# Performance work log

Measured on AMD Instinct MI355X. Metric: run time of the kernel, lower is better.

Reference implementation:

```python
import jax, jax.numpy as jnp
import numpy as np
from jax import lax

B, D, N, C = 8, 1, 12288, 256
H = 8            # num_heads
WS = 64          # window size (pixels per window)
HID = 1024       # mlp hidden = 4*C
K = 9            # conv kernel size
EPS = 1e-5


def setup_inputs() -> dict:
    key = jax.random.key(0)
    ks = jax.random.split(key, 8)
    w = lambda i, shape: jax.random.normal(ks[i], shape, jnp.float32) * 0.02
    return {
        "x": jax.random.normal(ks[0], (B, D, N, C), jnp.float32),
        "ln1_g": jnp.ones((C,), jnp.float32),
        "ln1_b": jnp.zeros((C,), jnp.float32),
        "conv_w": w(1, (C, C, K)),            # OIH layout (out_ch, in_ch, k)
        "conv_b": jnp.zeros((C,), jnp.float32),
        "qkv_w": w(2, (C, 3 * C)),            # stored (in, out): y = x @ W + b
        "qkv_b": jnp.zeros((3 * C,), jnp.float32),
        "proj_w": w(3, (C, C)),
        "proj_b": jnp.zeros((C,), jnp.float32),
        "ln2_g": jnp.ones((C,), jnp.float32),
        "ln2_b": jnp.zeros((C,), jnp.float32),
        "fc1_w": w(4, (C, HID)),
        "fc1_b": jnp.zeros((HID,), jnp.float32),
        "fc2_w": w(5, (HID, C)),
        "fc2_b": jnp.zeros((C,), jnp.float32),
    }


def _layernorm(x, g, b):
    mu = jnp.mean(x, axis=-1, keepdims=True)
    var = jnp.mean(jnp.square(x - mu), axis=-1, keepdims=True)
    return (x - mu) * lax.rsqrt(var + EPS) * g + b


def reference(x, ln1_g, ln1_b, conv_w, conv_b, qkv_w, qkv_b,
              proj_w, proj_b, ln2_g, ln2_b, fc1_w, fc1_b, fc2_w, fc2_b):
    shortcut = x                                  # (B, D, N, C)
    h = _layernorm(x, ln1_g, ln1_b)

    # Conv1d over pixel dim N, channels C, same padding
    hc = h.reshape(B * D, N, C).transpose(0, 2, 1)            # (BD, C, N)
    hc = lax.conv_general_dilated(
        hc, conv_w, window_strides=(1,), padding=[((K - 1) // 2, (K - 1) // 2)],
        dimension_numbers=("NCH", "OIH", "NCH"))
    hc = hc + conv_b[None, :, None]
    h = hc.transpose(0, 2, 1).reshape(B, D, N, C)

    # Window partition (no shift): (B*D*N/WS, WS, C)
    win = h.reshape(-1, WS, C)
    hd = C // H
    qkv = (win @ qkv_w + qkv_b).reshape(-1, WS, 3, H, hd)
    q = qkv[:, :, 0].transpose(0, 2, 1, 3)        # (nW, H, WS, hd)
    k = qkv[:, :, 1].transpose(0, 2, 1, 3)
    v = qkv[:, :, 2].transpose(0, 2, 1, 3)
    scale = hd ** (-0.5)
    attn = jnp.einsum("whqd,whkd->whqk", q * scale, k)
    attn = jax.nn.softmax(attn, axis=-1)
    out = jnp.einsum("whqk,whkd->whqd", attn, v)
    out = out.transpose(0, 2, 1, 3).reshape(-1, WS, C)
    out = out @ proj_w + proj_b

    h = out.reshape(B, D, N, C)
    x1 = shortcut + h                             # residual 1
    mlp_in = _layernorm(x1, ln2_g, ln2_b)
    mlp = jax.nn.gelu(mlp_in @ fc1_w + fc1_b, approximate=False) @ fc2_w + fc2_b
    return x1 + mlp                               # residual 2
```

## Files before the change

### kernel.cpp

```cpp
#include <hip/hip_runtime.h>

#define DEVI __device__ __forceinline__

typedef __attribute__((ext_vector_type(4))) float  f32x4;
typedef __attribute__((ext_vector_type(8))) short  s16x8;
typedef __attribute__((ext_vector_type(4))) short  s16x4;
typedef __attribute__((ext_vector_type(8))) __bf16 bf16x8;

constexpr int  Nn  = 12288;
constexpr int  NP  = 12296;
constexpr long TOK = 98304;

DEVI short f2bf(float f) {
  unsigned u = __builtin_bit_cast(unsigned, f);
  u += 0x7fffu + ((u >> 16) & 1u);
  return (short)(u >> 16);
}

DEVI f32x4 MFMA(s16x8 a, s16x8 b, f32x4 c) {
  return __builtin_amdgcn_mfma_f32_16x16x32_bf16(
      __builtin_bit_cast(bf16x8, a), __builtin_bit_cast(bf16x8, b), c, 0, 0, 0);
}

DEVI void gld16(const void* g, void* l) {
  __builtin_amdgcn_global_load_lds(
      (const __attribute__((address_space(1))) void*)g,
      (__attribute__((address_space(3))) void*)l, 16, 0, 0);
}

template <int CNT, int NT>
DEVI void stageG(const short* __restrict__ g_base, long g_row0, int ld, int k0,
                 short* __restrict__ lds, int tid) {
  const int w = tid >> 6;
#pragma unroll
  for (int c = 0; c < CNT; ++c) {
    const int u = c * NT + tid;
    const int row = u >> 3, ch = u & 7;
    const short* g = g_base + (g_row0 + row) * (long)ld + k0 + ch * 8;
    gld16(g, lds + (c * NT + w * 64) * 8);
  }
}

DEVI void xcd_decode(int W, int total, int ncol, long& row0, int& col0) {
  const int per = total >> 3;
  const int L = (W & 7) * per + (W >> 3);
  row0 = (long)(L / ncol) * 128;
  col0 = (L % ncol) * 128;
}

__global__ void prep_k(const float* __restrict__ qkv_w, const float* __restrict__ proj_w,
                       const float* __restrict__ fc1_w, const float* __restrict__ fc2_w,
                       const float* __restrict__ conv_w,
                       short* __restrict__ qkvWt, short* __restrict__ projWt,
                       short* __restrict__ fc1Wt, short* __restrict__ fc2Wt,
                       short* __restrict__ convWt, short* __restrict__ hp) {
  int idx = blockIdx.x * 256 + threadIdx.x;
  if (idx < 196608) {
    int o = idx >> 8, i = idx & 255;
    qkvWt[idx] = f2bf(qkv_w[i * 768 + o]);
    return;
  }
  idx -= 196608;
  if (idx < 65536) {
    int o = idx >> 8, i = idx & 255;
    projWt[idx] = f2bf(proj_w[i * 256 + o]);
    return;
  }
  idx -= 65536;
  if (idx < 262144) {
    int o = idx >> 8, i = idx & 255;
    fc1Wt[idx] = f2bf(fc1_w[i * 1024 + o]);
    return;
  }
  idx -= 262144;
  if (idx < 262144) {
    int o = idx >> 10, i = idx & 1023;
    fc2Wt[idx] = f2bf(fc2_w[i * 256 + o]);
    return;
  }
  idx -= 262144;
  if (idx < 589824) {
    int co = idx / 2304, rem = idx % 2304;
    int k = rem >> 8, ci = rem & 255;
    convWt[idx] = f2bf(conv_w[co * 2304 + ci * 9 + k]);
    return;
  }
  idx -= 589824;
  if (idx < 16384) {
    int b = idx >> 11, rem = idx & 2047;
    int rs = rem >> 8, ch = rem & 255;
    int p = rs < 4 ? rs : 12288 + rs;
    hp[((long)b * NP + p) * 256 + ch] = 0;
  }
}

__global__ __launch_bounds__(256) void ln_k(const float* __restrict__ x,
                                            const float* __restrict__ gw,
                                            const float* __restrict__ bw,
                                            short* __restrict__ out) {
  const int tid = threadIdx.x, w = tid >> 6, lane = tid & 63;
  const long t = (long)blockIdx.x * 4 + w;
  f32x4 v = *((const f32x4*)(x + t * 256) + lane);
  float s  = v[0] + v[1] + v[2] + v[3];
  float ss = v[0] * v[0] + v[1] * v[1] + v[2] * v[2] + v[3] * v[3];
#pragma unroll
  for (int mk = 1; mk < 64; mk <<= 1) {
    s  += __shfl_xor(s, mk);
    ss += __shfl_xor(ss, mk);
  }
  const float mu   = s * (1.0f / 256.0f);
  const float var  = ss * (1.0f / 256.0f) - mu * mu;
  const float rstd = rsqrtf(var + 1e-5f);
  f32x4 g4 = *((const f32x4*)gw + lane);
  f32x4 b4 = *((const f32x4*)bw + lane);
  const long orow = t + (t / Nn) * 8 + 4;
  s16x4 o4;
#pragma unroll
  for (int j = 0; j < 4; ++j) o4[j] = f2bf((v[j] - mu) * rstd * g4[j] + b4[j]);
  *((s16x4*)(out + orow * 256) + lane) = o4;
}

template <int EPI>
__global__ __launch_bounds__(256, 2) void gemm_k(
    const short* __restrict__ A, int lda,
    const short* __restrict__ Bt,
    const float* __restrict__ bias,
    const float* res, short* outS, float* outF,
    int ldo, int K, int ncol) {
  __shared__ __align__(16) short As[2][128][64];
  __shared__ __align__(16) short Bs[2][128][64];
  const int tid = threadIdx.x, w = tid >> 6, lane = tid & 63;
  const int q = lane >> 4, r16 = lane & 15;
  long row0; int col0;
  xcd_decode(blockIdx.x, gridDim.x, ncol, row0, col0);
  const int wr = w >> 1, wc = w & 1;
  f32x4 acc[4][4] = {};

  stageG<4, 256>(A, row0, lda, 0, &As[0][0][0], tid);
  stageG<4, 256>(Bt, col0, K, 0, &Bs[0][0][0], tid);
  __syncthreads();
  int cur = 0;
  for (int k0 = 0; k0 < K; k0 += 64) {
    if (k0 + 64 < K) {
      stageG<4, 256>(A, row0, lda, k0 + 64, &As[cur ^ 1][0][0], tid);
      stageG<4, 256>(Bt, col0, K, k0 + 64, &Bs[cur ^ 1][0][0], tid);
    }
#pragma unroll
    for (int kk = 0; kk < 2; ++kk) {
      s16x8 af[4], bfv[4];
#pragma unroll
      for (int m = 0; m < 4; ++m) af[m] = *(const s16x8*)&As[cur][wr * 64 + m * 16 + r16][kk * 32 + q * 8];
#pragma unroll
      for (int n = 0; n < 4; ++n) bfv[n] = *(const s16x8*)&Bs[cur][wc * 64 + n * 16 + r16][kk * 32 + q * 8];
#pragma unroll
      for (int m = 0; m < 4; ++m)
#pragma unroll
        for (int n = 0; n < 4; ++n) acc[m][n] = MFMA(af[m], bfv[n], acc[m][n]);
    }
    __syncthreads();
    cur ^= 1;
  }

  const long orow = row0 + wr * 64;
  const int  ocol = col0 + wc * 64;
#pragma unroll
  for (int n = 0; n < 4; ++n) {
    const int   gc = ocol + n * 16 + r16;
    const float bn = bias[gc];
#pragma unroll
    for (int m = 0; m < 4; ++m) {
      const long gr = orow + m * 16 + q * 4;
#pragma unroll
      for (int r = 0; r < 4; ++r) {
        float v = acc[m][n][r] + bn;
        const long o = (gr + r) * (long)ldo + gc;
        if constexpr (EPI == 0) {
          outS[o] = f2bf(v);
        } else if constexpr (EPI == 1) {
          outF[o] = v + res[o];
        } else {
          float t = 0.5f * v * (1.0f + erff(v * 0.70710678118654752f));
          outS[o] = f2bf(t);
        }
      }
    }
  }
}

__global__ __launch_bounds__(256, 2) void conv_k(const short* __restrict__ hp,
                                                 const short* __restrict__ convWt,
                                                 const float* __restrict__ bias,
                                                 short* __restrict__ out) {
  __shared__ __align__(16) short As[160][64];
  __shared__ __align__(16) short Bs[2][128][64];
  const int tid = threadIdx.x, w = tid >> 6, lane = tid & 63;
  const int q = lane >> 4, r16 = lane & 15;
  long row0; int col0;
  xcd_decode(blockIdx.x, gridDim.x, 2, row0, col0);
  const int  b  = (int)(row0 / Nn);
  const int  n0 = (int)(row0 % Nn);
  const long abase = (long)b * NP + n0;
  const int  wr = w >> 1, wc = w & 1;
  f32x4 acc[4][4] = {};

  stageG<5, 256>(hp, abase, 256, 0, &As[0][0], tid);
  stageG<4, 256>(convWt, col0, 2304, 0, &Bs[0][0][0], tid);
  __syncthreads();
  int cur = 0;
  for (int k0 = 0; k0 < 256; k0 += 64) {
    for (int tap = 0; tap < 9; ++tap) {
      if (tap < 8)
        stageG<4, 256>(convWt, col0, 2304, (tap + 1) * 256 + k0, &Bs[cur ^ 1][0][0], tid);
      else if (k0 + 64 < 256)
        stageG<4, 256>(convWt, col0, 2304, k0 + 64, &Bs[cur ^ 1][0][0], tid);
#pragma unroll
      for (int kk = 0; kk < 2; ++kk) {
        s16x8 af[4], bfv[4];
#pragma unroll
        for (int m = 0; m < 4; ++m)
          af[m] = *(const s16x8*)&As[tap + wr * 64 + m * 16 + r16][kk * 32 + q * 8];
#pragma unroll
        for (int n = 0; n < 4; ++n)
          bfv[n] = *(const s16x8*)&Bs[cur][wc * 64 + n * 16 + r16][kk * 32 + q * 8];
#pragma unroll
        for (int m = 0; m < 4; ++m)
#pragma unroll
          for (int n = 0; n < 4; ++n) acc[m][n] = MFMA(af[m], bfv[n], acc[m][n]);
      }
      __syncthreads();
      cur ^= 1;
    }
    if (k0 + 64 < 256) {
      stageG<5, 256>(hp, abase, 256, k0 + 64, &As[0][0], tid);
      __syncthreads();
    }
  }

  const long orow = row0 + wr * 64;
  const int  ocol = col0 + wc * 64;
#pragma unroll
  for (int n = 0; n < 4; ++n) {
    const int   gc = ocol + n * 16 + r16;
    const float bn = bias[gc];
#pragma unroll
    for (int m = 0; m < 4; ++m) {
      const long gr = orow + m * 16 + q * 4;
#pragma unroll
      for (int r = 0; r < 4; ++r) out[(gr + r) * 256L + gc] = f2bf(acc[m][n][r] + bn);
    }
  }
}

__global__ __launch_bounds__(512, 4) void proj_ln_k(
    const short* __restrict__ A,
    const short* __restrict__ Bt,
    const float* __restrict__ bias,
    const float* __restrict__ res,
    const float* __restrict__ gw, const float* __restrict__ bw,
    float* __restrict__ x1,
    short* __restrict__ lnout) {
  __shared__ __align__(16) short As[128][64];
  __shared__ __align__(16) short Bs[256][64];
  __shared__ float red[4][128][2];
  const int tid = threadIdx.x, w = tid >> 6, lane = tid & 63;
  const int q = lane >> 4, r16 = lane & 15;
  const int W = blockIdx.x, per = gridDim.x >> 3;
  const long row0 = (long)((W & 7) * per + (W >> 3)) * 128;
  const int wr = w >> 2, wc = w & 3;
  f32x4 acc[4][4] = {};

  for (int k0 = 0; k0 < 256; k0 += 64) {
    stageG<2, 512>(A, row0, 256, k0, &As[0][0], tid);
    stageG<4, 512>(Bt, 0, 256, k0, &Bs[0][0], tid);
    __syncthreads();
#pragma unroll
    for (int kk = 0; kk < 2; ++kk) {
      s16x8 af[4], bfv[4];
#pragma unroll
      for (int m = 0; m < 4; ++m) af[m] = *(const s16x8*)&As[wr * 64 + m * 16 + r16][kk * 32 + q * 8];
#pragma unroll
      for (int n = 0; n < 4; ++n) bfv[n] = *(const s16x8*)&Bs[wc * 64 + n * 16 + r16][kk * 32 + q * 8];
#pragma unroll
      for (int m = 0; m < 4; ++m)
#pragma unroll
        for (int n = 0; n < 4; ++n) acc[m][n] = MFMA(af[m], bfv[n], acc[m][n]);
    }
    __syncthreads();
  }

  float biasr[4], gv[4], bv[4];
#pragma unroll
  for (int n = 0; n < 4; ++n) {
    const int gc = wc * 64 + n * 16 + r16;
    biasr[n] = bias[gc]; gv[n] = gw[gc]; bv[n] = bw[gc];
  }

#pragma unroll
  for (int m = 0; m < 4; ++m) {
#pragma unroll
    for (int r = 0; r < 4; ++r) {
      const long gr = row0 + wr * 64 + m * 16 + q * 4 + r;
      float s = 0.f, ss = 0.f;
#pragma unroll
      for (int n = 0; n < 4; ++n) {
        const int gc = wc * 64 + n * 16 + r16;
        float v = acc[m][n][r] + biasr[n] + res[gr * 256 + gc];
        acc[m][n][r] = v;
        x1[gr * 256 + gc] = v;
        s += v; ss += v * v;
      }
#pragma unroll
      for (int mk = 1; mk < 16; mk <<= 1) {
        s  += __shfl_xor(s, mk);
        ss += __shfl_xor(ss, mk);
      }
      if (r16 == 0) {
        const int lr = wr * 64 + m * 16 + q * 4 + r;
        red[wc][lr][0] = s;
        red[wc][lr][1] = ss;
      }
    }
  }
  __syncthreads();

#pragma unroll
  for (int m = 0; m < 4; ++m) {
#pragma unroll
    for (int r = 0; r < 4; ++r) {
      const int  lr = wr * 64 + m * 16 + q * 4 + r;
      const long gr = row0 + lr;
      const float S  = red[0][lr][0] + red[1][lr][0] + red[2][lr][0] + red[3][lr][0];
      const float SS = red[0][lr][1] + red[1][lr][1] + red[2][lr][1] + red[3][lr][1];
      const float mu = S * (1.0f / 256.0f);
      const float rstd = rsqrtf(SS * (1.0f / 256.0f) - mu * mu + 1e-5f);
#pragma unroll
      for (int n = 0; n < 4; ++n) {
        const int gc = wc * 64 + n * 16 + r16;
        lnout[gr * 256 + gc] = f2bf((acc[m][n][r] - mu) * rstd * gv[n] + bv[n]);
      }
    }
  }
}

__global__ __launch_bounds__(256, 2) void attn_k(const short* __restrict__ qkv,
                                                 short* __restrict__ o) {
  __shared__ __align__(16) short Pt[4][64][68];
  __shared__ __align__(16) short Vs[4][64][32];
  const int tid = threadIdx.x, w = tid >> 6, lane = tid & 63;
  const int q = lane >> 4, r16 = lane & 15;
  const int job = blockIdx.x * 4 + w;
  const int win = job >> 3, h = job & 7;
  const short* base = qkv + (long)win * 64 * 768;

#pragma unroll
  for (int c = 0; c < 4; ++c) {
    const int idx16 = c * 64 + lane;
    const short* g = base + (long)(idx16 >> 2) * 768 + 512 + h * 32 + (idx16 & 3) * 8;
    gld16(g, (char*)&Vs[w][0][0] + c * 1024);
  }

  s16x8 aq[4], bk[4];
#pragma unroll
  for (int m = 0; m < 4; ++m)
    aq[m] = *(const s16x8*)(base + (long)(m * 16 + r16) * 768 + h * 32 + q * 8);
#pragma unroll
  for (int n = 0; n < 4; ++n)
    bk[n] = *(const s16x8*)(base + (long)(n * 16 + r16) * 768 + 256 + h * 32 + q * 8);
  f32x4 sc[4][4] = {};
#pragma unroll
  for (int m = 0; m < 4; ++m)
#pragma unroll
    for (int n = 0; n < 4; ++n) sc[m][n] = MFMA(aq[m], bk[n], sc[m][n]);

  const float scale = 0.17677669529663687f;
#pragma unroll
  for (int m = 0; m < 4; ++m) {
#pragma unroll
    for (int r = 0; r < 4; ++r) {
      float a0 = sc[m][0][r] * scale, a1 = sc[m][1][r] * scale;
      float a2 = sc[m][2][r] * scale, a3 = sc[m][3][r] * scale;
      float mx = fmaxf(fmaxf(a0, a1), fmaxf(a2, a3));
      mx = fmaxf(mx, __shfl_xor(mx, 1));
      mx = fmaxf(mx, __shfl_xor(mx, 2));
      mx = fmaxf(mx, __shfl_xor(mx, 4));
      mx = fmaxf(mx, __shfl_xor(mx, 8));
      float e0 = __expf(a0 - mx), e1 = __expf(a1 - mx);
      float e2 = __expf(a2 - mx), e3 = __expf(a3 - mx);
      float sm = e0 + e1 + e2 + e3;
      sm += __shfl_xor(sm, 1);
      sm += __shfl_xor(sm, 2);
      sm += __shfl_xor(sm, 4);
      sm += __shfl_xor(sm, 8);
      float inv = 1.0f / sm;
      sc[m][0][r] = e0 * inv; sc[m][1][r] = e1 * inv;
      sc[m][2][r] = e2 * inv; sc[m][3][r] = e3 * inv;
    }
  }

#pragma unroll
  for (int m = 0; m < 4; ++m)
#pragma unroll
    for (int n = 0; n < 4; ++n) {
      s16x4 p4;
#pragma unroll
      for (int r = 0; r < 4; ++r) p4[r] = f2bf(sc[m][n][r]);
      *(s16x4*)&Pt[w][n * 16 + r16][m * 16 + q * 4] = p4;
    }

  asm volatile("s_waitcnt vmcnt(0)" ::: "memory");

  f32x4 oa[4][2] = {};
#pragma unroll
  for (int ks = 0; ks < 2; ++ks) {
    s16x8 bv[2];
#pragma unroll
    for (int nt = 0; nt < 2; ++nt)
#pragma unroll
      for (int jj = 0; jj < 8; ++jj)
        bv[nt][jj] = Vs[w][ks * 32 + q * 8 + jj][nt * 16 + r16];
#pragma unroll
    for (int m = 0; m < 4; ++m) {
      s16x8 ap;
#pragma unroll
      for (int jj = 0; jj < 8; ++jj)
        ap[jj] = Pt[w][ks * 32 + q * 8 + jj][m * 16 + r16];
#pragma unroll
      for (int nt = 0; nt < 2; ++nt) oa[m][nt] = MFMA(ap, bv[nt], oa[m][nt]);
    }
  }

  short* ob = o + (long)win * 64 * 256 + h * 32;
#pragma unroll
  for (int m = 0; m < 4; ++m)
#pragma unroll
    for (int nt = 0; nt < 2; ++nt)
#pragma unroll
      for (int r = 0; r < 4; ++r)
        ob[(long)(m * 16 + q * 4 + r) * 256 + nt * 16 + r16] = f2bf(oa[m][nt][r]);
}

extern "C" void kernel_launch(void* const* d_in, const int* in_sizes, int n_in,
                              void* d_out, int out_size, void* d_ws, size_t ws_size,
                              hipStream_t stream) {
  const float* x      = (const float*)d_in[0];
  const float* ln1_g  = (const float*)d_in[1];
  const float* ln1_b  = (const float*)d_in[2];
  const float* conv_w = (const float*)d_in[3];
  const float* conv_b = (const float*)d_in[4];
  const float* qkv_w  = (const float*)d_in[5];
  const float* qkv_b  = (const float*)d_in[6];
  const float* proj_w = (const float*)d_in[7];
  const float* proj_b = (const float*)d_in[8];
  const float* ln2_g  = (const float*)d_in[9];
  const float* ln2_b  = (const float*)d_in[10];
  const float* fc1_w  = (const float*)d_in[11];
  const float* fc1_b  = (const float*)d_in[12];
  const float* fc2_w  = (const float*)d_in[13];
  const float* fc2_b  = (const float*)d_in[14];
  float* out = (float*)d_out;

  constexpr long HPsz = (long)8 * NP * 256;
  constexpr long Qsz  = TOK * 768;
  constexpr long Csz  = TOK * 256;
  short* ws    = (short*)d_ws;
  short* hp    = ws;
  short* qkvB  = ws + HPsz;
  short* cvB   = ws + HPsz + Qsz;
  short* hidB  = qkvB;
  short* wts   = ws + HPsz + Qsz + Csz;
  short* qkvWt  = wts;
  short* projWt = qkvWt + 196608;
  short* fc1Wt  = projWt + 65536;
  short* fc2Wt  = fc1Wt + 262144;
  short* convWt = fc2Wt + 262144;

  prep_k<<<5440, 256, 0, stream>>>(qkv_w, proj_w, fc1_w, fc2_w, conv_w,
                                   qkvWt, projWt, fc1Wt, fc2Wt, convWt, hp);
  ln_k<<<24576, 256, 0, stream>>>(x, ln1_g, ln1_b, hp);
  conv_k<<<1536, 256, 0, stream>>>(hp, convWt, conv_b, cvB);
  gemm_k<0><<<4608, 256, 0, stream>>>(cvB, 256, qkvWt, qkv_b,
                                      nullptr, qkvB, nullptr, 768, 256, 6);
  attn_k<<<3072, 256, 0, stream>>>(qkvB, hp);
  proj_ln_k<<<768, 512, 0, stream>>>(hp, projWt, proj_b, x, ln2_g, ln2_b, out, hp);
  gemm_k<2><<<6144, 256, 0, stream>>>(hp, 256, fc1Wt, fc1_b,
                                      nullptr, hidB, nullptr, 1024, 256, 8);
  gemm_k<1><<<1536, 256, 0, stream>>>(hidB, 1024, fc2Wt, fc2_b,
                                      out, nullptr, out, 256, 1024, 2);
}
```

Baseline: 722.5 us.

## Add weight-stationary GEMM for K=256 projections and single-buffer generic GEMM

Adds a weight-stationary GEMM kernel that loads a column slice of the weight matrix (K=256) into swizzled LDS once per block. It then loops over many row tiles, reading A fragments directly from global memory into registers. The kernel replaces the tiled GEMM for the qkv and fc1 projections, which removes repeated weight staging and per-k-step barriers. The remaining fc2 GEMM drops double buffering to free LDS, at the risk of exposing global-load latency. Reading A straight from global memory without LDS staging may give uncoalesced or latency-bound access.

```diff
diff --git a/kernel.cpp b/kernel.cpp
--- a/kernel.cpp
+++ b/kernel.cpp
@@ -120,6 +120,67 @@
   *((s16x4*)(out + orow * 256) + lane) = o4;
 }
 
+template <int NFH, int EPI>
+__global__ __launch_bounds__(256, 2) void wgemm_k(
+    const short* __restrict__ A, const short* __restrict__ Bt,
+    const float* __restrict__ bias, short* __restrict__ outS,
+    const int ldo, const int bps, const int iters) {
+  constexpr int NS = NFH * 32;
+  __shared__ __align__(16) short Wl[NS * 256];
+  const int tid = threadIdx.x, w = tid >> 6, lane = tid & 63;
+  const int q = lane >> 4, r16 = lane & 15, e = r16 & 7;
+  const int slice = blockIdx.x / bps, gb = blockIdx.x % bps;
+  const int col0 = slice * NS;
+
+  for (int u = tid; u < NS * 32; u += 256) {
+    const int row = u >> 5, ul = u & 31;
+    s16x8 v = *(const s16x8*)(Bt + (long)(col0 + row) * 256 + ul * 8);
+    *(s16x8*)(Wl + row * 256 + ((ul ^ ((row & 7) << 2)) * 8)) = v;
+  }
+  __syncthreads();
+
+  for (int i = 0; i < iters; ++i) {
+    const long row0 = ((long)(gb + i * bps) * 4 + w) * 64;
+    const short* aB[4];
+#pragma unroll
+    for (int m = 0; m < 4; ++m) aB[m] = A + (row0 + m * 16 + r16) * 256 + q * 8;
+#pragma unroll
+    for (int half = 0; half < 2; ++half) {
+      const int dsb = half * NFH * 4096 + r16 * 256 + q * 8;
+      f32x4 acc[4][NFH] = {};
+#pragma unroll
+      for (int kk = 0; kk < 8; ++kk) {
+        s16x8 af[4];
+#pragma unroll
+        for (int m = 0; m < 4; ++m) af[m] = *(const s16x8*)(aB[m] + kk * 32);
+        const short* bp = Wl + dsb + ((kk ^ e) << 5);
+#pragma unroll
+        for (int nf = 0; nf < NFH; ++nf) {
+          s16x8 bfr = *(const s16x8*)(bp + nf * 4096);
+#pragma unroll
+          for (int m = 0; m < 4; ++m) acc[m][nf] = MFMA(af[m], bfr, acc[m][nf]);
+        }
+      }
+#pragma unroll
+      for (int nf = 0; nf < NFH; ++nf) {
+        const int gc = col0 + (half * NFH + nf) * 16 + r16;
+        const float bn = bias[gc];
+#pragma unroll
+        for (int m = 0; m < 4; ++m) {
+          const long gr = row0 + m * 16 + q * 4;
+#pragma unroll
+          for (int r = 0; r < 4; ++r) {
+            float v = acc[m][nf][r] + bn;
+            if constexpr (EPI == 2)
+              v = 0.5f * v * (1.0f + erff(v * 0.70710678118654752f));
+            outS[(gr + r) * (long)ldo + gc] = f2bf(v);
+          }
+        }
+      }
+    }
+  }
+}
+
 template <int EPI>
 __global__ __launch_bounds__(256, 2) void gemm_k(
     const short* __restrict__ A, int lda,
@@ -127,8 +188,8 @@
     const float* __restrict__ bias,
     const float* res, short* outS, float* outF,
     int ldo, int K, int ncol) {
-  __shared__ __align__(16) short As[2][128][64];
-  __shared__ __align__(16) short Bs[2][128][64];
+  __shared__ __align__(16) short As[128][64];
+  __shared__ __align__(16) short Bs[128][64];
   const int tid = threadIdx.x, w = tid >> 6, lane = tid & 63;
   const int q = lane >> 4, r16 = lane & 15;
   long row0; int col0;
@@ -136,29 +197,23 @@
   const int wr = w >> 1, wc = w & 1;
   f32x4 acc[4][4] = {};
 
-  stageG<4, 256>(A, row0, lda, 0, &As[0][0][0], tid);
-  stageG<4, 256>(Bt, col0, K, 0, &Bs[0][0][0], tid);
-  __syncthreads();
-  int cur = 0;
   for (int k0 = 0; k0 < K; k0 += 64) {
-    if (k0 + 64 < K) {
-      stageG<4, 256>(A, row0, lda, k0 + 64, &As[cur ^ 1][0][0], tid);
-      stageG<4, 256>(Bt, col0, K, k0 + 64, &Bs[cur ^ 1][0][0], tid);
-    }
+    stageG<4, 256>(A, row0, lda, k0, &As[0][0], tid);
+    stageG<4, 256>(Bt, col0, K, k0, &Bs[0][0], tid);
+    __syncthreads();
 #pragma unroll
     for (int kk = 0; kk < 2; ++kk) {
       s16x8 af[4], bfv[4];
 #pragma unroll
-      for (int m = 0; m < 4; ++m) af[m] = *(const s16x8*)&As[cur][wr * 64 + m * 16 + r16][kk * 32 + q * 8];
-#pragma unroll
-      for (int n = 0; n < 4; ++n) bfv[n] = *(const s16x8*)&Bs[cur][wc * 64 + n * 16 + r16][kk * 32 + q * 8];
+      for (int m = 0; m < 4; ++m) af[m] = *(const s16x8*)&As[wr * 64 + m * 16 + r16][kk * 32 + q * 8];
+#pragma unroll
+      for (int n = 0; n < 4; ++n) bfv[n] = *(const s16x8*)&Bs[wc * 64 + n * 16 + r16][kk * 32 + q * 8];
 #pragma unroll
       for (int m = 0; m < 4; ++m)
 #pragma unroll
         for (int n = 0; n < 4; ++n) acc[m][n] = MFMA(af[m], bfv[n], acc[m][n]);
     }
     __syncthreads();
-    cur ^= 1;
   }
 
   const long orow = row0 + wr * 64;
@@ -478,12 +533,10 @@
                                    qkvWt, projWt, fc1Wt, fc2Wt, convWt, hp);
   ln_k<<<24576, 256, 0, stream>>>(x, ln1_g, ln1_b, hp);
   conv_k<<<1536, 256, 0, stream>>>(hp, convWt, conv_b, cvB);
-  gemm_k<0><<<4608, 256, 0, stream>>>(cvB, 256, qkvWt, qkv_b,
-                                      nullptr, qkvB, nullptr, 768, 256, 6);
+  wgemm_k<3, 0><<<512, 256, 0, stream>>>(cvB, qkvWt, qkv_b, qkvB, 768, 64, 6);
   attn_k<<<3072, 256, 0, stream>>>(qkvB, hp);
   proj_ln_k<<<768, 512, 0, stream>>>(hp, projWt, proj_b, x, ln2_g, ln2_b, out, hp);
-  gemm_k<2><<<6144, 256, 0, stream>>>(hp, 256, fc1Wt, fc1_b,
-                                      nullptr, hidB, nullptr, 1024, 256, 8);
+  wgemm_k<4, 2><<<512, 256, 0, stream>>>(hp, fc1Wt, fc1_b, hidB, 1024, 64, 6);
   gemm_k<1><<<1536, 256, 0, stream>>>(hidB, 1024, fc2Wt, fc2_b,
                                       out, nullptr, out, 256, 1024, 2);
 }
```

New measurement: 734.4 us. Within noise of the previous version (+1.6%).

## Replace tiled GEMM with weight-stationary persistent GEMM reading A from global

Applied to the files above, without the earlier changes.

Replaces the double-buffered LDS-tiled GEMM with a persistent weight-stationary kernel. Each block loads a column slice of the weight matrix into XOR-swizzled LDS once, then loops over many 64-row A tiles per wave, loading A fragments straight from global memory. This removes repeated weight staging and the per-k-step barriers. In exchange, A loads are uncoalesced per-lane 16-byte reads with no LDS reuse across column slices, and far fewer blocks are launched. The fc2 GEMM holds a 64x1024 weight slice (128 KB) in LDS per block, which may limit occupancy.

```diff
diff --git a/kernel.cpp b/kernel.cpp
--- a/kernel.cpp
+++ b/kernel.cpp
@@ -120,67 +120,65 @@
   *((s16x4*)(out + orow * 256) + lane) = o4;
 }
 
-template <int EPI>
-__global__ __launch_bounds__(256, 2) void gemm_k(
-    const short* __restrict__ A, int lda,
-    const short* __restrict__ Bt,
-    const float* __restrict__ bias,
-    const float* res, short* outS, float* outF,
-    int ldo, int K, int ncol) {
-  __shared__ __align__(16) short As[2][128][64];
-  __shared__ __align__(16) short Bs[2][128][64];
+template <int NF, int K, int WAVES, int EPI>
+__global__ __launch_bounds__(WAVES * 64, 2) void wgemm_k(
+    const short* __restrict__ A, const short* __restrict__ Bt,
+    const float* __restrict__ bias, const float* __restrict__ res,
+    short* __restrict__ outS, float* __restrict__ outF,
+    const int ldo, const int bps, const int iters) {
+  constexpr int NS  = NF * 16;
+  constexpr int UPR = K / 8;
+  __shared__ __align__(16) short Wl[NS * K];
   const int tid = threadIdx.x, w = tid >> 6, lane = tid & 63;
-  const int q = lane >> 4, r16 = lane & 15;
-  long row0; int col0;
-  xcd_decode(blockIdx.x, gridDim.x, ncol, row0, col0);
-  const int wr = w >> 1, wc = w & 1;
-  f32x4 acc[4][4] = {};
-
-  stageG<4, 256>(A, row0, lda, 0, &As[0][0][0], tid);
-  stageG<4, 256>(Bt, col0, K, 0, &Bs[0][0][0], tid);
+  const int q = lane >> 4, r16 = lane & 15, e = r16 & 7;
+  const int slice = blockIdx.x / bps, gb = blockIdx.x % bps;
+  const int col0 = slice * NS;
+
+  for (int u = tid; u < NS * UPR; u += WAVES * 64) {
+    const int row = u / UPR, ul = u % UPR;
+    s16x8 v = *(const s16x8*)(Bt + (long)(col0 + row) * K + ul * 8);
+    *(s16x8*)(Wl + row * K + ((ul ^ ((row & 7) << 2)) * 8)) = v;
+  }
   __syncthreads();
-  int cur = 0;
-  for (int k0 = 0; k0 < K; k0 += 64) {
-    if (k0 + 64 < K) {
-      stageG<4, 256>(A, row0, lda, k0 + 64, &As[cur ^ 1][0][0], tid);
-      stageG<4, 256>(Bt, col0, K, k0 + 64, &Bs[cur ^ 1][0][0], tid);
-    }
-#pragma unroll
-    for (int kk = 0; kk < 2; ++kk) {
-      s16x8 af[4], bfv[4];
-#pragma unroll
-      for (int m = 0; m < 4; ++m) af[m] = *(const s16x8*)&As[cur][wr * 64 + m * 16 + r16][kk * 32 + q * 8];
-#pragma unroll
-      for (int n = 0; n < 4; ++n) bfv[n] = *(const s16x8*)&Bs[cur][wc * 64 + n * 16 + r16][kk * 32 + q * 8];
-#pragma unroll
-      for (int m = 0; m < 4; ++m)
-#pragma unroll
-        for (int n = 0; n < 4; ++n) acc[m][n] = MFMA(af[m], bfv[n], acc[m][n]);
-    }
-    __syncthreads();
-    cur ^= 1;
-  }
-
-  const long orow = row0 + wr * 64;
-  const int  ocol = col0 + wc * 64;
-#pragma unroll
-  for (int n = 0; n < 4; ++n) {
-    const int   gc = ocol + n * 16 + r16;
-    const float bn = bias[gc];
-#pragma unroll
-    for (int m = 0; m < 4; ++m) {
-      const long gr = orow + m * 16 + q * 4;
-#pragma unroll
-      for (int r = 0; r < 4; ++r) {
-        float v = acc[m][n][r] + bn;
-        const long o = (gr + r) * (long)ldo + gc;
-        if constexpr (EPI == 0) {
-          outS[o] = f2bf(v);
-        } else if constexpr (EPI == 1) {
-          outF[o] = v + res[o];
-        } else {
-          float t = 0.5f * v * (1.0f + erff(v * 0.70710678118654752f));
-          outS[o] = f2bf(t);
+
+  for (int i = 0; i < iters; ++i) {
+    const long row0 = ((long)(gb + i * bps) * WAVES + w) * 64;
+    const short* aB[4];
+#pragma unroll
+    for (int m = 0; m < 4; ++m) aB[m] = A + (row0 + m * 16 + r16) * (long)K + q * 8;
+    f32x4 acc[4][NF] = {};
+#pragma unroll
+    for (int kk = 0; kk < K / 32; ++kk) {
+      s16x8 af[4];
+#pragma unroll
+      for (int m = 0; m < 4; ++m) af[m] = *(const s16x8*)(aB[m] + kk * 32);
+      const short* bp = Wl + r16 * K + q * 8 + ((kk ^ e) << 5);
+#pragma unroll
+      for (int nf = 0; nf < NF; ++nf) {
+        s16x8 bfr = *(const s16x8*)(bp + nf * 16 * K);
+#pragma unroll
+        for (int m = 0; m < 4; ++m) acc[m][nf] = MFMA(af[m], bfr, acc[m][nf]);
+      }
+    }
+#pragma unroll
+    for (int nf = 0; nf < NF; ++nf) {
+      const int gc = col0 + nf * 16 + r16;
+      const float bn = bias[gc];
+#pragma unroll
+      for (int m = 0; m < 4; ++m) {
+        const long gr = row0 + m * 16 + q * 4;
+#pragma unroll
+        for (int r = 0; r < 4; ++r) {
+          float v = acc[m][nf][r] + bn;
+          const long o = (gr + r) * (long)ldo + gc;
+          if constexpr (EPI == 0) {
+            outS[o] = f2bf(v);
+          } else if constexpr (EPI == 1) {
+            outF[o] = v + res[o];
+          } else {
+            float t = 0.5f * v * (1.0f + erff(v * 0.70710678118654752f));
+            outS[o] = f2bf(t);
+          }
         }
       }
     }
@@ -478,12 +476,12 @@
                                    qkvWt, projWt, fc1Wt, fc2Wt, convWt, hp);
   ln_k<<<24576, 256, 0, stream>>>(x, ln1_g, ln1_b, hp);
   conv_k<<<1536, 256, 0, stream>>>(hp, convWt, conv_b, cvB);
-  gemm_k<0><<<4608, 256, 0, stream>>>(cvB, 256, qkvWt, qkv_b,
-                                      nullptr, qkvB, nullptr, 768, 256, 6);
+  wgemm_k<6, 256, 4, 0><<<512, 256, 0, stream>>>(cvB, qkvWt, qkv_b, nullptr,
+                                                 qkvB, nullptr, 768, 64, 6);
   attn_k<<<3072, 256, 0, stream>>>(qkvB, hp);
   proj_ln_k<<<768, 512, 0, stream>>>(hp, projWt, proj_b, x, ln2_g, ln2_b, out, hp);
-  gemm_k<2><<<6144, 256, 0, stream>>>(hp, 256, fc1Wt, fc1_b,
-                                      nullptr, hidB, nullptr, 1024, 256, 8);
-  gemm_k<1><<<1536, 256, 0, stream>>>(hidB, 1024, fc2Wt, fc2_b,
-                                      out, nullptr, out, 256, 1024, 2);
-}
+  wgemm_k<8, 256, 4, 2><<<512, 256, 0, stream>>>(hp, fc1Wt, fc1_b, nullptr,
+                                                 hidB, nullptr, 1024, 64, 6);
+  wgemm_k<4, 1024, 8, 1><<<256, 512, 0, stream>>>(hidB, fc2Wt, fc2_b, out,
+                                                  nullptr, out, 256, 64, 3);
+}
```

Result: slower. 993.2 us (+37.5%).

## Replace 128x128 double-buffered GEMM with 256x256 single-buffered 512-thread tile

Applied to the files above, without the earlier changes.

The GEMM kernel now uses 256x256 output tiles computed by 8 waves (each 128x64). This roughly halves global and LDS traffic per MFMA and reuses each A fragment across four B fragments. The double buffering is dropped, so loads are no longer overlapped with compute and every k-step pays two barriers. The XCD block remap is replaced by an inline version. The fc2 GEMM now launches only 384 blocks, which risks poor occupancy given the higher register use.

```diff
diff --git a/kernel.cpp b/kernel.cpp
--- a/kernel.cpp
+++ b/kernel.cpp
@@ -121,54 +121,51 @@
 }
 
 template <int EPI>
-__global__ __launch_bounds__(256, 2) void gemm_k(
+__global__ __launch_bounds__(512, 2) void gemm256_k(
     const short* __restrict__ A, int lda,
     const short* __restrict__ Bt,
     const float* __restrict__ bias,
     const float* res, short* outS, float* outF,
     int ldo, int K, int ncol) {
-  __shared__ __align__(16) short As[2][128][64];
-  __shared__ __align__(16) short Bs[2][128][64];
+  __shared__ __align__(16) short As[256][64];
+  __shared__ __align__(16) short Bs[256][64];
   const int tid = threadIdx.x, w = tid >> 6, lane = tid & 63;
   const int q = lane >> 4, r16 = lane & 15;
-  long row0; int col0;
-  xcd_decode(blockIdx.x, gridDim.x, ncol, row0, col0);
-  const int wr = w >> 1, wc = w & 1;
-  f32x4 acc[4][4] = {};
-
-  stageG<4, 256>(A, row0, lda, 0, &As[0][0][0], tid);
-  stageG<4, 256>(Bt, col0, K, 0, &Bs[0][0][0], tid);
-  __syncthreads();
-  int cur = 0;
+  const int W = blockIdx.x, per = gridDim.x >> 3;
+  const int L = (W & 7) * per + (W >> 3);
+  const long row0 = (long)(L / ncol) * 256;
+  const int  col0 = (L % ncol) * 256;
+  const int wr = w >> 2, wc = w & 3;
+  f32x4 acc[8][4] = {};
+
   for (int k0 = 0; k0 < K; k0 += 64) {
-    if (k0 + 64 < K) {
-      stageG<4, 256>(A, row0, lda, k0 + 64, &As[cur ^ 1][0][0], tid);
-      stageG<4, 256>(Bt, col0, K, k0 + 64, &Bs[cur ^ 1][0][0], tid);
-    }
+    stageG<4, 512>(A, row0, lda, k0, &As[0][0], tid);
+    stageG<4, 512>(Bt, col0, K, k0, &Bs[0][0], tid);
+    __syncthreads();
 #pragma unroll
     for (int kk = 0; kk < 2; ++kk) {
-      s16x8 af[4], bfv[4];
-#pragma unroll
-      for (int m = 0; m < 4; ++m) af[m] = *(const s16x8*)&As[cur][wr * 64 + m * 16 + r16][kk * 32 + q * 8];
-#pragma unroll
-      for (int n = 0; n < 4; ++n) bfv[n] = *(const s16x8*)&Bs[cur][wc * 64 + n * 16 + r16][kk * 32 + q * 8];
-#pragma unroll
-      for (int m = 0; m < 4; ++m)
-#pragma unroll
-        for (int n = 0; n < 4; ++n) acc[m][n] = MFMA(af[m], bfv[n], acc[m][n]);
+      s16x8 bfv[4];
+#pragma unroll
+      for (int n = 0; n < 4; ++n)
+        bfv[n] = *(const s16x8*)&Bs[wc * 64 + n * 16 + r16][kk * 32 + q * 8];
+#pragma unroll
+      for (int m = 0; m < 8; ++m) {
+        s16x8 af = *(const s16x8*)&As[wr * 128 + m * 16 + r16][kk * 32 + q * 8];
+#pragma unroll
+        for (int n = 0; n < 4; ++n) acc[m][n] = MFMA(af, bfv[n], acc[m][n]);
+      }
     }
     __syncthreads();
-    cur ^= 1;
-  }
-
-  const long orow = row0 + wr * 64;
+  }
+
+  const long orow = row0 + wr * 128;
   const int  ocol = col0 + wc * 64;
 #pragma unroll
   for (int n = 0; n < 4; ++n) {
     const int   gc = ocol + n * 16 + r16;
     const float bn = bias[gc];
 #pragma unroll
-    for (int m = 0; m < 4; ++m) {
+    for (int m = 0; m < 8; ++m) {
       const long gr = orow + m * 16 + q * 4;
 #pragma unroll
       for (int r = 0; r < 4; ++r) {
@@ -478,12 +475,12 @@
                                    qkvWt, projWt, fc1Wt, fc2Wt, convWt, hp);
   ln_k<<<24576, 256, 0, stream>>>(x, ln1_g, ln1_b, hp);
   conv_k<<<1536, 256, 0, stream>>>(hp, convWt, conv_b, cvB);
-  gemm_k<0><<<4608, 256, 0, stream>>>(cvB, 256, qkvWt, qkv_b,
-                                      nullptr, qkvB, nullptr, 768, 256, 6);
+  gemm256_k<0><<<1152, 512, 0, stream>>>(cvB, 256, qkvWt, qkv_b,
+                                         nullptr, qkvB, nullptr, 768, 256, 3);
   attn_k<<<3072, 256, 0, stream>>>(qkvB, hp);
   proj_ln_k<<<768, 512, 0, stream>>>(hp, projWt, proj_b, x, ln2_g, ln2_b, out, hp);
-  gemm_k<2><<<6144, 256, 0, stream>>>(hp, 256, fc1Wt, fc1_b,
-                                      nullptr, hidB, nullptr, 1024, 256, 8);
-  gemm_k<1><<<1536, 256, 0, stream>>>(hidB, 1024, fc2Wt, fc2_b,
-                                      out, nullptr, out, 256, 1024, 2);
-}
+  gemm256_k<2><<<1536, 512, 0, stream>>>(hp, 256, fc1Wt, fc1_b,
+                                         nullptr, hidB, nullptr, 1024, 256, 4);
+  gemm256_k<1><<<384, 512, 0, stream>>>(hidB, 1024, fc2Wt, fc2_b,
+                                        out, nullptr, out, 256, 1024, 1);
+}
```

New measurement: 833.7 us. +15.4%, slower.
